# Kernel tuning notes

Measured on AMD Instinct MI355X. Metric: run time of the kernel, lower is better.

Reference implementation:

```python
import jax, jax.numpy as jnp
import numpy as np

D_IN = 1024
D_OUT = 1024
NUM_HEADS = 16
HEAD_DIM = D_OUT // NUM_HEADS


def setup_inputs() -> dict:
    key = jax.random.key(0)
    kx, kq, kk, kv, ko = jax.random.split(key, 5)
    s = 1.0 / np.sqrt(D_IN)
    return {
        "x": jax.random.normal(kx, (1, 4096, D_IN), dtype=jnp.float32),
        "Wq": jax.random.normal(kq, (D_IN, D_OUT), dtype=jnp.float32) * s,
        "Wk": jax.random.normal(kk, (D_IN, D_OUT), dtype=jnp.float32) * s,
        "Wv": jax.random.normal(kv, (D_IN, D_OUT), dtype=jnp.float32) * s,
        "Wo": jax.random.normal(ko, (D_OUT, D_OUT), dtype=jnp.float32) * s,
    }


def reference(x, Wq, Wk, Wv, Wo):
    b, s, _ = x.shape
    # project and split heads: [b, h, s, d]
    def split_heads(t):
        return t.reshape(b, s, NUM_HEADS, HEAD_DIM).transpose(0, 2, 1, 3)
    Q = split_heads(x @ Wq)
    K = split_heads(x @ Wk)
    V = split_heads(x @ Wv)
    scores = jnp.einsum("bhqd,bhkd->bhqk", Q, K) / jnp.sqrt(jnp.float32(HEAD_DIM))
    causal = jnp.triu(jnp.ones((s, s), dtype=bool), k=1)  # True above diagonal
    scores = jnp.where(causal, -jnp.inf, scores)
    probs = jax.nn.softmax(scores, axis=-1)
    out = jnp.einsum("bhqk,bhkd->bhqd", probs, V)
    out = out.transpose(0, 2, 1, 3).reshape(b, s, D_OUT)
    return out @ Wo
```

## Files before the change

### kernel.cpp

```cpp
#include <hip/hip_runtime.h>
#include <cstdint>

#define S_LEN 4096
#define D_MODEL 1024
#define NHEAD 16
#define HDIM 64

typedef __bf16 bf16_t;
typedef __bf16 bf16x8 __attribute__((ext_vector_type(8)));
typedef __bf16 bf16x4 __attribute__((ext_vector_type(4)));
typedef float floatx4 __attribute__((ext_vector_type(4)));

#define QSCALE 0.18033688011112042f

__device__ __forceinline__ void lds_cp16(void* lds, const void* g) {
    __builtin_amdgcn_global_load_lds(
        (const __attribute__((address_space(1))) unsigned int*)g,
        (__attribute__((address_space(3))) unsigned int*)lds,
        16, 0, 0);
}

__device__ __forceinline__ float fast_exp2(float x) {
    float r;
    asm("v_exp_f32 %0, %1" : "=v"(r) : "v"(x));
    return r;
}

__global__ __launch_bounds__(256) void k_prep(const float* __restrict__ x,
                                              const float* __restrict__ Wq,
                                              const float* __restrict__ Wk,
                                              const float* __restrict__ Wv,
                                              const float* __restrict__ Wo,
                                              bf16_t* __restrict__ xb,
                                              bf16_t* __restrict__ WtQKV,
                                              bf16_t* __restrict__ WtO) {
    const int bx = blockIdx.x;
    if (bx < 4096) {
        int i = bx * 256 + threadIdx.x;
        float4 v = ((const float4*)x)[i];
        bf16x4 o;
        o[0] = (bf16_t)v.x; o[1] = (bf16_t)v.y; o[2] = (bf16_t)v.z; o[3] = (bf16_t)v.w;
        *(bf16x4*)(xb + (size_t)i * 4) = o;
        return;
    }
    __shared__ float lds[64][65];
    const int i = bx - 4096;
    const int z = i >> 8, rem = i & 255;
    const float* W = (z == 0) ? Wq : (z == 1) ? Wk : (z == 2) ? Wv : Wo;
    bf16_t* Wt = (z < 3) ? (WtQKV + (size_t)z * 1048576) : WtO;
    const int k0 = (rem >> 4) * 64, n0 = (rem & 15) * 64;
    const int t = threadIdx.x, cl = t & 63, rl = t >> 6;
#pragma unroll
    for (int r = 0; r < 16; ++r)
        lds[r * 4 + rl][cl] = W[(size_t)(k0 + r * 4 + rl) * 1024 + n0 + cl];
    __syncthreads();
#pragma unroll
    for (int r = 0; r < 16; ++r)
        Wt[(size_t)(n0 + r * 4 + rl) * 1024 + k0 + cl] = (bf16_t)lds[cl][r * 4 + rl];
}

template <int MODE, int MT>
__global__ __launch_bounds__(256) void k_gemm(const bf16_t* __restrict__ A,
                                              const bf16_t* __restrict__ Bt,
                                              float* __restrict__ Cout,
                                              bf16_t* __restrict__ Qb,
                                              bf16_t* __restrict__ Kb,
                                              bf16_t* __restrict__ Vt) {
    constexpr int MI = MT / 32;
    __shared__ __align__(16) bf16_t sA[MT * 32];
    __shared__ __align__(16) bf16_t sB[128 * 32];
    const int t = threadIdx.x, w = t >> 6, lane = t & 63, quad = lane >> 4, l15 = lane & 15;
    const int m0 = blockIdx.x * MT, n0 = blockIdx.y * 128;
    const int wm = w >> 1, wn = w & 1;

    floatx4 acc[MI][4];
#pragma unroll
    for (int i = 0; i < MI; ++i)
#pragma unroll
        for (int j = 0; j < 4; ++j)
            acc[i][j] = floatx4{0.f, 0.f, 0.f, 0.f};

    for (int kb = 0; kb < 32; ++kb) {
        __syncthreads();
#pragma unroll
        for (int r = 0; r < MT / 64; ++r) {
            int c = t + 256 * r;
            int row = c >> 2, kq = c & 3;
            lds_cp16(&sA[w * 512 + r * 2048],
                     A + (size_t)(m0 + row) * 1024 + kb * 32 + kq * 8);
        }
#pragma unroll
        for (int r = 0; r < 2; ++r) {
            int c = t + 256 * r;
            int row = c >> 2, kq = c & 3;
            lds_cp16(&sB[w * 512 + r * 2048],
                     Bt + (size_t)(n0 + row) * 1024 + kb * 32 + kq * 8);
        }
        __syncthreads();
        bf16x8 af[MI], bfr[4];
#pragma unroll
        for (int i = 0; i < MI; ++i)
            af[i] = *(const bf16x8*)&sA[(wm * (MT / 2) + i * 16 + l15) * 32 + quad * 8];
#pragma unroll
        for (int j = 0; j < 4; ++j)
            bfr[j] = *(const bf16x8*)&sB[(wn * 64 + j * 16 + l15) * 32 + quad * 8];
#pragma unroll
        for (int i = 0; i < MI; ++i)
#pragma unroll
            for (int j = 0; j < 4; ++j)
                acc[i][j] = __builtin_amdgcn_mfma_f32_16x16x32_bf16(af[i], bfr[j],
                                                                    acc[i][j], 0, 0, 0);
    }

    const int mrow = m0 + wm * (MT / 2) + quad * 4;
    if (MODE == 0) {
        const int ncol = n0 + wn * 64 + l15;
#pragma unroll
        for (int i = 0; i < MI; ++i)
#pragma unroll
            for (int j = 0; j < 4; ++j)
#pragma unroll
                for (int r = 0; r < 4; ++r)
                    Cout[(size_t)(mrow + i * 16 + r) * 1024 + ncol + j * 16] = acc[i][j][r];
    } else {
        const int g = (int)blockIdx.y >> 3;
        const int ncbase = ((int)blockIdx.y & 7) * 128 + wn * 64 + l15;
        if (g == 2) {
#pragma unroll
            for (int j = 0; j < 4; ++j) {
                int nc = ncbase + j * 16;
                int hh = nc >> 6, dd = nc & 63;
                bf16_t* dst = Vt + (size_t)hh * 262144 + (size_t)dd * 64;
#pragma unroll
                for (int i = 0; i < MI; ++i) {
                    int s0r = mrow + i * 16;
                    bf16x4 pk;
                    pk[0] = (bf16_t)acc[i][j][0]; pk[1] = (bf16_t)acc[i][j][1];
                    pk[2] = (bf16_t)acc[i][j][2]; pk[3] = (bf16_t)acc[i][j][3];
                    int kk = s0r & 63;
                    int pp = (kk & 0x20) | ((kk & 0xC) << 1) | ((kk & 0x10) >> 2);
                    *(bf16x4*)&dst[(size_t)(s0r >> 6) * 4096 + pp] = pk;
                }
            }
        } else {
            bf16_t* base = g ? Kb : Qb;
            const float sc = g ? 1.0f : QSCALE;
#pragma unroll
            for (int j = 0; j < 4; ++j) {
                int nc = ncbase + j * 16;
                int hh = nc >> 6, dd = nc & 63;
#pragma unroll
                for (int i = 0; i < MI; ++i)
#pragma unroll
                    for (int r = 0; r < 4; ++r)
                        base[(size_t)hh * 262144 + (size_t)(mrow + i * 16 + r) * 64 + dd] =
                            (bf16_t)(acc[i][j][r] * sc);
            }
        }
    }
}

__global__ __launch_bounds__(256, 4) void k_attn(const bf16_t* __restrict__ Qb,
                                                 const bf16_t* __restrict__ Kb,
                                                 const bf16_t* __restrict__ Vt,
                                                 bf16_t* __restrict__ OP0,
                                                 bf16_t* __restrict__ OP1,
                                                 float* __restrict__ Lp) {
    __shared__ __align__(16) bf16_t Ks[2][64 * 64];
    __shared__ __align__(16) bf16_t Vts[2][64 * 64];
    const int bid = blockIdx.x;
    const int slot = bid >> 8, jj = bid & 255, g = jj >> 5, u = jj & 31;
    const int h = u >> 1, sp = u & 1;
    const int qb = (slot == 0) ? (31 - g) : (slot == 1) ? (16 + g)
                 : (slot == 2) ? (15 - g) : g;
    const int t = threadIdx.x, w = t >> 6, quad = (t & 63) >> 4, l15 = t & 15;
    const bf16_t* Qh = Qb + (size_t)h * 262144;
    const bf16_t* Kh = Kb + (size_t)h * 262144;
    const bf16_t* Vth = Vt + (size_t)h * 262144;

    const bf16_t* Qrow = Qh + (size_t)(qb * 128 + w * 32 + l15) * 64;
    bf16x8 bq[2][2];
#pragma unroll
    for (int qt = 0; qt < 2; ++qt)
#pragma unroll
        for (int kh = 0; kh < 2; ++kh)
            bq[qt][kh] = *(const bf16x8*)(Qrow + qt * 1024 + kh * 32 + quad * 8);

    float l_s[2] = {0.f, 0.f};
    floatx4 o_acc[2][4];
#pragma unroll
    for (int qt = 0; qt < 2; ++qt)
#pragma unroll
        for (int j = 0; j < 4; ++j) o_acc[qt][j] = floatx4{0.f, 0.f, 0.f, 0.f};

#define STAGE_K(b, kb_)                                                            \
    {                                                                              \
        _Pragma("unroll") for (int r = 0; r < 2; ++r) {                            \
            int c = t + 256 * r;                                                   \
            int row = c >> 3, sw = (c & 7) ^ (row & 7);                            \
            lds_cp16(&Ks[b][c * 8], Kh + (size_t)(kb_) * 4096 + row * 64 + sw * 8);\
        }                                                                          \
    }
#define STAGE_V(b, kb_)                                                            \
    {                                                                              \
        _Pragma("unroll") for (int r = 0; r < 2; ++r) {                            \
            int c = t + 256 * r;                                                   \
            int row = c >> 3, sw = (c & 7) ^ (row & 7);                            \
            lds_cp16(&Vts[b][c * 8], Vth + (size_t)(kb_) * 4096 + row * 64 + sw * 8);\
        }                                                                          \
    }

    const int t0 = sp ? (qb + 1) : 0;
    const int nIter = qb + 1;
    const int qmax = qb * 128 + w * 32 + 31;

    STAGE_K(0, t0)
    STAGE_V(0, t0)
    for (int it = 0; it < nIter; ++it) {
        const int kb = t0 + it;
        const int buf = it & 1;
        __syncthreads();
        if (it + 1 < nIter) {
            STAGE_K(buf ^ 1, kb + 1)
            STAGE_V(buf ^ 1, kb + 1)
        }
        const bool active = (kb * 64 <= qmax);

        if (active) {
            floatx4 st[2][4];
            __builtin_amdgcn_s_setprio(1);
#pragma unroll
            for (int j = 0; j < 4; ++j) {
                int rk = j * 16 + l15;
                bf16x8 a0 = *(const bf16x8*)&Ks[buf][rk * 64 + ((quad ^ (rk & 7)) * 8)];
                bf16x8 a1 = *(const bf16x8*)&Ks[buf][rk * 64 + (((quad + 4) ^ (rk & 7)) * 8)];
#pragma unroll
                for (int qt = 0; qt < 2; ++qt) {
                    floatx4 z = {0.f, 0.f, 0.f, 0.f};
                    st[qt][j] = __builtin_amdgcn_mfma_f32_16x16x32_bf16(a0, bq[qt][0], z, 0, 0, 0);
                    st[qt][j] = __builtin_amdgcn_mfma_f32_16x16x32_bf16(a1, bq[qt][1], st[qt][j], 0, 0, 0);
                }
            }
            __builtin_amdgcn_s_setprio(0);
            if (kb >= 2 * qb) {
#pragma unroll
                for (int qt = 0; qt < 2; ++qt) {
                    int qg = qb * 128 + w * 32 + qt * 16 + l15;
#pragma unroll
                    for (int j = 0; j < 4; ++j)
#pragma unroll
                        for (int r = 0; r < 4; ++r) {
                            int keyg = kb * 64 + j * 16 + quad * 4 + r;
                            if (keyg > qg) st[qt][j][r] = -1e30f;
                        }
                }
            }
            bf16x8 pa[2][2];
#pragma unroll
            for (int qt = 0; qt < 2; ++qt) {
                float a0 = 0.f, a1 = 0.f, a2 = 0.f, a3 = 0.f;
#pragma unroll
                for (int j = 0; j < 4; ++j) {
                    st[qt][j][0] = fast_exp2(st[qt][j][0]); a0 += st[qt][j][0];
                    st[qt][j][1] = fast_exp2(st[qt][j][1]); a1 += st[qt][j][1];
                    st[qt][j][2] = fast_exp2(st[qt][j][2]); a2 += st[qt][j][2];
                    st[qt][j][3] = fast_exp2(st[qt][j][3]); a3 += st[qt][j][3];
                }
                l_s[qt] += (a0 + a1) + (a2 + a3);
#pragma unroll
                for (int kh = 0; kh < 2; ++kh)
#pragma unroll
                    for (int m = 0; m < 4; ++m) {
                        pa[qt][kh][m]     = (bf16_t)st[qt][2 * kh][m];
                        pa[qt][kh][4 + m] = (bf16_t)st[qt][2 * kh + 1][m];
                    }
            }
            __builtin_amdgcn_s_setprio(1);
#pragma unroll
            for (int kh = 0; kh < 2; ++kh) {
                int pc = kh * 4 + quad;
#pragma unroll
                for (int j = 0; j < 4; ++j) {
                    int rd = j * 16 + l15;
                    bf16x8 bv = *(const bf16x8*)&Vts[buf][rd * 64 + ((pc ^ (rd & 7)) * 8)];
                    o_acc[0][j] = __builtin_amdgcn_mfma_f32_16x16x32_bf16(pa[0][kh], bv, o_acc[0][j], 0, 0, 0);
                    o_acc[1][j] = __builtin_amdgcn_mfma_f32_16x16x32_bf16(pa[1][kh], bv, o_acc[1][j], 0, 0, 0);
                }
            }
            __builtin_amdgcn_s_setprio(0);
        }
    }
    bf16_t* OPx = sp ? OP1 : OP0;
#pragma unroll
    for (int qt = 0; qt < 2; ++qt) {
        float l = l_s[qt];
        l += __shfl_xor(l, 16);
        l += __shfl_xor(l, 32);
        if (quad == 0)
            Lp[sp * 65536 + h * 4096 + (qb * 128 + w * 32 + qt * 16 + l15)] = l;
#pragma unroll
        for (int r = 0; r < 4; ++r) {
            int rowg = qb * 128 + w * 32 + qt * 16 + quad * 4 + r;
#pragma unroll
            for (int j = 0; j < 4; ++j)
                OPx[(size_t)rowg * 1024 + h * 64 + j * 16 + l15] = (bf16_t)o_acc[qt][j][r];
        }
    }
#undef STAGE_K
#undef STAGE_V
}

__global__ __launch_bounds__(256) void k_combine(const bf16_t* __restrict__ OP0,
                                                 const bf16_t* __restrict__ OP1,
                                                 const float* __restrict__ Lp,
                                                 bf16_t* __restrict__ Ob) {
    int gi = (blockIdx.x * 256 + threadIdx.x) * 4;
    int q = gi >> 10, hh = (gi & 1023) >> 6;
    float inv = 1.0f / (Lp[hh * 4096 + q] + Lp[65536 + hh * 4096 + q]);
    bf16x4 a = *(const bf16x4*)(OP0 + gi);
    bf16x4 b = *(const bf16x4*)(OP1 + gi);
    bf16x4 o;
#pragma unroll
    for (int r = 0; r < 4; ++r)
        o[r] = (bf16_t)(((float)a[r] + (float)b[r]) * inv);
    *(bf16x4*)(Ob + gi) = o;
}

extern "C" void kernel_launch(void* const* d_in, const int* in_sizes, int n_in,
                              void* d_out, int out_size, void* d_ws, size_t ws_size,
                              hipStream_t stream) {
    const float* x  = (const float*)d_in[0];
    const float* Wq = (const float*)d_in[1];
    const float* Wk = (const float*)d_in[2];
    const float* Wv = (const float*)d_in[3];
    const float* Wo = (const float*)d_in[4];

    bf16_t* ws = (bf16_t*)d_ws;
    bf16_t* Xb    = ws;
    bf16_t* WtQKV = Xb + 4194304;
    bf16_t* WtO   = WtQKV + 3145728;
    bf16_t* Qb    = WtO + 1048576;
    bf16_t* Kb    = Qb + 4194304;
    bf16_t* Vt    = Kb + 4194304;
    bf16_t* Ob    = Vt + 4194304;
    bf16_t* OP1   = Ob + 4194304;
    bf16_t* OP0   = Xb;
    float*  Lp    = (float*)WtQKV;
    float* out = (float*)d_out;

    k_prep<<<5120, 256, 0, stream>>>(x, Wq, Wk, Wv, Wo, Xb, WtQKV, WtO);
    k_gemm<1, 128><<<dim3(32, 24), 256, 0, stream>>>(Xb, WtQKV, nullptr, Qb, Kb, Vt);
    k_attn<<<1024, 256, 0, stream>>>(Qb, Kb, Vt, OP0, OP1, Lp);
    k_combine<<<4096, 256, 0, stream>>>(OP0, OP1, Lp, Ob);
    k_gemm<0, 64><<<dim3(64, 8), 256, 0, stream>>>(Ob, WtO, out, nullptr, nullptr, nullptr);
}
```

Before: 188.4 us.

## Fuse split-K combine into output GEMM and widen attention waves to 64 query rows

The separate combine kernel is removed: the output-projection GEMM now loads both partial attention outputs and the row sums per K-slice, normalizes them in registers and writes the bf16 tile into LDS, saving one launch and the Ob round-trip. Separately, the attention kernel drops to 128 threads per block, so each wave processes 64 query rows (4 tiles) instead of 32, reusing each K/V LDS fragment across more MFMAs. The cost is higher register pressure in attention, fewer waves per block for latency hiding, and synchronous global loads replacing async LDS copies for the A operand in the final GEMM.

```diff
diff --git a/kernel.cpp b/kernel.cpp
--- a/kernel.cpp
+++ b/kernel.cpp
@@ -65,7 +65,9 @@
                                               float* __restrict__ Cout,
                                               bf16_t* __restrict__ Qb,
                                               bf16_t* __restrict__ Kb,
-                                              bf16_t* __restrict__ Vt) {
+                                              bf16_t* __restrict__ Vt,
+                                              const bf16_t* __restrict__ OP1x,
+                                              const float* __restrict__ Lpx) {
     constexpr int MI = MT / 32;
     __shared__ __align__(16) bf16_t sA[MT * 32];
     __shared__ __align__(16) bf16_t sB[128 * 32];
@@ -80,14 +82,41 @@
         for (int j = 0; j < 4; ++j)
             acc[i][j] = floatx4{0.f, 0.f, 0.f, 0.f};
 
+    const int crow = m0 + (t >> 2), ckq = t & 3;
+    bf16x8 cA{}, cB{};
+    float cla = 0.f, clb = 0.f;
+    if (MODE == 2) {
+        cA = *(const bf16x8*)(A + (size_t)crow * 1024 + ckq * 8);
+        cB = *(const bf16x8*)(OP1x + (size_t)crow * 1024 + ckq * 8);
+        cla = Lpx[crow];
+        clb = Lpx[65536 + crow];
+    }
+
     for (int kb = 0; kb < 32; ++kb) {
         __syncthreads();
-#pragma unroll
-        for (int r = 0; r < MT / 64; ++r) {
-            int c = t + 256 * r;
-            int row = c >> 2, kq = c & 3;
-            lds_cp16(&sA[w * 512 + r * 2048],
-                     A + (size_t)(m0 + row) * 1024 + kb * 32 + kq * 8);
+        if (MODE == 2) {
+            float inv = __builtin_amdgcn_rcpf(cla + clb);
+            bf16x8 o;
+#pragma unroll
+            for (int e = 0; e < 8; ++e)
+                o[e] = (bf16_t)(((float)cA[e] + (float)cB[e]) * inv);
+            *(bf16x8*)&sA[t * 8] = o;
+            if (kb + 1 < 32) {
+                int h2 = (kb + 1) >> 1;
+                int col = (kb + 1) * 32 + ckq * 8;
+                cA = *(const bf16x8*)(A + (size_t)crow * 1024 + col);
+                cB = *(const bf16x8*)(OP1x + (size_t)crow * 1024 + col);
+                cla = Lpx[h2 * 4096 + crow];
+                clb = Lpx[65536 + h2 * 4096 + crow];
+            }
+        } else {
+#pragma unroll
+            for (int r = 0; r < MT / 64; ++r) {
+                int c = t + 256 * r;
+                int row = c >> 2, kq = c & 3;
+                lds_cp16(&sA[w * 512 + r * 2048],
+                         A + (size_t)(m0 + row) * 1024 + kb * 32 + kq * 8);
+            }
         }
 #pragma unroll
         for (int r = 0; r < 2; ++r) {
@@ -113,7 +142,7 @@
     }
 
     const int mrow = m0 + wm * (MT / 2) + quad * 4;
-    if (MODE == 0) {
+    if (MODE == 0 || MODE == 2) {
         const int ncol = n0 + wn * 64 + l15;
 #pragma unroll
         for (int i = 0; i < MI; ++i)
@@ -160,7 +189,7 @@
     }
 }
 
-__global__ __launch_bounds__(256, 4) void k_attn(const bf16_t* __restrict__ Qb,
+__global__ __launch_bounds__(128, 2) void k_attn(const bf16_t* __restrict__ Qb,
                                                  const bf16_t* __restrict__ Kb,
                                                  const bf16_t* __restrict__ Vt,
                                                  bf16_t* __restrict__ OP0,
@@ -178,33 +207,33 @@
     const bf16_t* Kh = Kb + (size_t)h * 262144;
     const bf16_t* Vth = Vt + (size_t)h * 262144;
 
-    const bf16_t* Qrow = Qh + (size_t)(qb * 128 + w * 32 + l15) * 64;
-    bf16x8 bq[2][2];
-#pragma unroll
-    for (int qt = 0; qt < 2; ++qt)
+    const bf16_t* Qrow = Qh + (size_t)(qb * 128 + w * 64 + l15) * 64;
+    bf16x8 bq[4][2];
+#pragma unroll
+    for (int qt = 0; qt < 4; ++qt)
 #pragma unroll
         for (int kh = 0; kh < 2; ++kh)
             bq[qt][kh] = *(const bf16x8*)(Qrow + qt * 1024 + kh * 32 + quad * 8);
 
-    float l_s[2] = {0.f, 0.f};
-    floatx4 o_acc[2][4];
-#pragma unroll
-    for (int qt = 0; qt < 2; ++qt)
+    float l_s[4] = {0.f, 0.f, 0.f, 0.f};
+    floatx4 o_acc[4][4];
+#pragma unroll
+    for (int qt = 0; qt < 4; ++qt)
 #pragma unroll
         for (int j = 0; j < 4; ++j) o_acc[qt][j] = floatx4{0.f, 0.f, 0.f, 0.f};
 
 #define STAGE_K(b, kb_)                                                            \
     {                                                                              \
-        _Pragma("unroll") for (int r = 0; r < 2; ++r) {                            \
-            int c = t + 256 * r;                                                   \
+        _Pragma("unroll") for (int r = 0; r < 4; ++r) {                            \
+            int c = t + 128 * r;                                                   \
             int row = c >> 3, sw = (c & 7) ^ (row & 7);                            \
             lds_cp16(&Ks[b][c * 8], Kh + (size_t)(kb_) * 4096 + row * 64 + sw * 8);\
         }                                                                          \
     }
 #define STAGE_V(b, kb_)                                                            \
     {                                                                              \
-        _Pragma("unroll") for (int r = 0; r < 2; ++r) {                            \
-            int c = t + 256 * r;                                                   \
+        _Pragma("unroll") for (int r = 0; r < 4; ++r) {                            \
+            int c = t + 128 * r;                                                   \
             int row = c >> 3, sw = (c & 7) ^ (row & 7);                            \
             lds_cp16(&Vts[b][c * 8], Vth + (size_t)(kb_) * 4096 + row * 64 + sw * 8);\
         }                                                                          \
@@ -212,7 +241,7 @@
 
     const int t0 = sp ? (qb + 1) : 0;
     const int nIter = qb + 1;
-    const int qmax = qb * 128 + w * 32 + 31;
+    const int qmax = qb * 128 + w * 64 + 63;
 
     STAGE_K(0, t0)
     STAGE_V(0, t0)
@@ -227,25 +256,28 @@
         const bool active = (kb * 64 <= qmax);
 
         if (active) {
-            floatx4 st[2][4];
-            __builtin_amdgcn_s_setprio(1);
+            bf16x8 ak[4][2];
 #pragma unroll
             for (int j = 0; j < 4; ++j) {
                 int rk = j * 16 + l15;
-                bf16x8 a0 = *(const bf16x8*)&Ks[buf][rk * 64 + ((quad ^ (rk & 7)) * 8)];
-                bf16x8 a1 = *(const bf16x8*)&Ks[buf][rk * 64 + (((quad + 4) ^ (rk & 7)) * 8)];
-#pragma unroll
-                for (int qt = 0; qt < 2; ++qt) {
+                ak[j][0] = *(const bf16x8*)&Ks[buf][rk * 64 + ((quad ^ (rk & 7)) * 8)];
+                ak[j][1] = *(const bf16x8*)&Ks[buf][rk * 64 + (((quad + 4) ^ (rk & 7)) * 8)];
+            }
+            floatx4 st[4][4];
+            __builtin_amdgcn_s_setprio(1);
+#pragma unroll
+            for (int j = 0; j < 4; ++j)
+#pragma unroll
+                for (int qt = 0; qt < 4; ++qt) {
                     floatx4 z = {0.f, 0.f, 0.f, 0.f};
-                    st[qt][j] = __builtin_amdgcn_mfma_f32_16x16x32_bf16(a0, bq[qt][0], z, 0, 0, 0);
-                    st[qt][j] = __builtin_amdgcn_mfma_f32_16x16x32_bf16(a1, bq[qt][1], st[qt][j], 0, 0, 0);
-                }
-            }
+                    st[qt][j] = __builtin_amdgcn_mfma_f32_16x16x32_bf16(ak[j][0], bq[qt][0], z, 0, 0, 0);
+                    st[qt][j] = __builtin_amdgcn_mfma_f32_16x16x32_bf16(ak[j][1], bq[qt][1], st[qt][j], 0, 0, 0);
+                }
             __builtin_amdgcn_s_setprio(0);
             if (kb >= 2 * qb) {
 #pragma unroll
-                for (int qt = 0; qt < 2; ++qt) {
-                    int qg = qb * 128 + w * 32 + qt * 16 + l15;
+                for (int qt = 0; qt < 4; ++qt) {
+                    int qg = qb * 128 + w * 64 + qt * 16 + l15;
 #pragma unroll
                     for (int j = 0; j < 4; ++j)
 #pragma unroll
@@ -255,9 +287,9 @@
                         }
                 }
             }
-            bf16x8 pa[2][2];
-#pragma unroll
-            for (int qt = 0; qt < 2; ++qt) {
+            bf16x8 pa[4][2];
+#pragma unroll
+            for (int qt = 0; qt < 4; ++qt) {
                 float a0 = 0.f, a1 = 0.f, a2 = 0.f, a3 = 0.f;
 #pragma unroll
                 for (int j = 0; j < 4; ++j) {
@@ -283,8 +315,9 @@
                 for (int j = 0; j < 4; ++j) {
                     int rd = j * 16 + l15;
                     bf16x8 bv = *(const bf16x8*)&Vts[buf][rd * 64 + ((pc ^ (rd & 7)) * 8)];
-                    o_acc[0][j] = __builtin_amdgcn_mfma_f32_16x16x32_bf16(pa[0][kh], bv, o_acc[0][j], 0, 0, 0);
-                    o_acc[1][j] = __builtin_amdgcn_mfma_f32_16x16x32_bf16(pa[1][kh], bv, o_acc[1][j], 0, 0, 0);
+#pragma unroll
+                    for (int qt = 0; qt < 4; ++qt)
+                        o_acc[qt][j] = __builtin_amdgcn_mfma_f32_16x16x32_bf16(pa[qt][kh], bv, o_acc[qt][j], 0, 0, 0);
                 }
             }
             __builtin_amdgcn_s_setprio(0);
@@ -292,15 +325,15 @@
     }
     bf16_t* OPx = sp ? OP1 : OP0;
 #pragma unroll
-    for (int qt = 0; qt < 2; ++qt) {
+    for (int qt = 0; qt < 4; ++qt) {
         float l = l_s[qt];
         l += __shfl_xor(l, 16);
         l += __shfl_xor(l, 32);
         if (quad == 0)
-            Lp[sp * 65536 + h * 4096 + (qb * 128 + w * 32 + qt * 16 + l15)] = l;
+            Lp[sp * 65536 + h * 4096 + (qb * 128 + w * 64 + qt * 16 + l15)] = l;
 #pragma unroll
         for (int r = 0; r < 4; ++r) {
-            int rowg = qb * 128 + w * 32 + qt * 16 + quad * 4 + r;
+            int rowg = qb * 128 + w * 64 + qt * 16 + quad * 4 + r;
 #pragma unroll
             for (int j = 0; j < 4; ++j)
                 OPx[(size_t)rowg * 1024 + h * 64 + j * 16 + l15] = (bf16_t)o_acc[qt][j][r];
@@ -308,22 +341,6 @@
     }
 #undef STAGE_K
 #undef STAGE_V
-}
-
-__global__ __launch_bounds__(256) void k_combine(const bf16_t* __restrict__ OP0,
-                                                 const bf16_t* __restrict__ OP1,
-                                                 const float* __restrict__ Lp,
-                                                 bf16_t* __restrict__ Ob) {
-    int gi = (blockIdx.x * 256 + threadIdx.x) * 4;
-    int q = gi >> 10, hh = (gi & 1023) >> 6;
-    float inv = 1.0f / (Lp[hh * 4096 + q] + Lp[65536 + hh * 4096 + q]);
-    bf16x4 a = *(const bf16x4*)(OP0 + gi);
-    bf16x4 b = *(const bf16x4*)(OP1 + gi);
-    bf16x4 o;
-#pragma unroll
-    for (int r = 0; r < 4; ++r)
-        o[r] = (bf16_t)(((float)a[r] + (float)b[r]) * inv);
-    *(bf16x4*)(Ob + gi) = o;
 }
 
 extern "C" void kernel_launch(void* const* d_in, const int* in_sizes, int n_in,
@@ -342,15 +359,15 @@
     bf16_t* Qb    = WtO + 1048576;
     bf16_t* Kb    = Qb + 4194304;
     bf16_t* Vt    = Kb + 4194304;
-    bf16_t* Ob    = Vt + 4194304;
-    bf16_t* OP1   = Ob + 4194304;
+    bf16_t* OP1   = Vt + 4194304;
     bf16_t* OP0   = Xb;
     float*  Lp    = (float*)WtQKV;
     float* out = (float*)d_out;
 
     k_prep<<<5120, 256, 0, stream>>>(x, Wq, Wk, Wv, Wo, Xb, WtQKV, WtO);
-    k_gemm<1, 128><<<dim3(32, 24), 256, 0, stream>>>(Xb, WtQKV, nullptr, Qb, Kb, Vt);
-    k_attn<<<1024, 256, 0, stream>>>(Qb, Kb, Vt, OP0, OP1, Lp);
-    k_combine<<<4096, 256, 0, stream>>>(OP0, OP1, Lp, Ob);
-    k_gemm<0, 64><<<dim3(64, 8), 256, 0, stream>>>(Ob, WtO, out, nullptr, nullptr, nullptr);
-}
+    k_gemm<1, 128><<<dim3(32, 24), 256, 0, stream>>>(Xb, WtQKV, nullptr, Qb, Kb, Vt,
+                                                     nullptr, nullptr);
+    k_attn<<<1024, 128, 0, stream>>>(Qb, Kb, Vt, OP0, OP1, Lp);
+    k_gemm<2, 64><<<dim3(64, 8), 256, 0, stream>>>(OP0, WtO, out, nullptr, nullptr,
+                                                   nullptr, OP1, Lp);
+}
```

Result: slower. 199.7 us (+6.0%).
